# Kernel optimization log

Measured on AMD Instinct MI355X. Metric: run time of the kernel, lower is better.

## Reference

```python
import jax, jax.numpy as jnp
import numpy as np

EPS = 1e-6
N_HEADS = 128
QK_NOPE = 128
QK_ROPE = 64
KV_RANK = 512

def rmsnorm(x, gamma):
    var = jnp.mean(jnp.square(x), axis=-1, keepdims=True)
    return x * jax.lax.rsqrt(var + EPS) * gamma

def apply_rope(x, cos, sin):
    # x: [..., D], cos/sin broadcastable to x; rotate-half convention
    x1, x2 = jnp.split(x, 2, axis=-1)
    rot = jnp.concatenate([-x2, x1], axis=-1)
    return x * cos + rot * sin

def setup_inputs() -> dict:
    key = jax.random.key(0)
    ks = jax.random.split(key, 6)
    T, H = 4096, 7168
    inp = {
        "token_x": jax.random.normal(ks[0], (T, H), jnp.float32),
        "wq_a": jax.random.normal(ks[1], (H, 1536), jnp.float32) * 0.02,
        "wq_b": jax.random.normal(ks[2], (1536, N_HEADS * (QK_NOPE + QK_ROPE)), jnp.float32) * 0.02,
        "wkv": jax.random.normal(ks[3], (H, KV_RANK + QK_ROPE), jnp.float32) * 0.02,
        "rope_cos": jax.random.uniform(ks[4], (T, QK_ROPE), jnp.float32, -1.0, 1.0),
        "rope_sin": jax.random.uniform(ks[5], (T, QK_ROPE), jnp.float32, -1.0, 1.0),
        "gamma_cq": jnp.ones((1536,), jnp.float32),
        "gamma_ckv": jnp.ones((KV_RANK,), jnp.float32),
    }
    return inp

def reference(token_x, wq_a, wq_b, wkv, rope_cos, rope_sin, gamma_cq, gamma_ckv):
    T = token_x.shape[0]
    # Query path: down-proj -> RMSNorm -> up-proj -> split -> RoPE on rope part
    cq = rmsnorm(token_x @ wq_a, gamma_cq)                    # [T, 1536]
    q = (cq @ wq_b).reshape(T, N_HEADS, QK_NOPE + QK_ROPE)    # [T, H, 192]
    q_nope, q_rope = q[..., :QK_NOPE], q[..., QK_NOPE:]
    q_rope = apply_rope(q_rope, rope_cos[:, None, :], rope_sin[:, None, :])
    query = jnp.concatenate([q_nope, q_rope], axis=-1)        # [T, H, 192]
    # KV path: joint down-proj -> split latent / rope-key -> RMSNorm + RoPE
    kv = token_x @ wkv                                        # [T, 576]
    ckv = rmsnorm(kv[:, :KV_RANK], gamma_ckv)                 # [T, 512]
    k_rope = apply_rope(kv[:, KV_RANK:], rope_cos, rope_sin)  # [T, 64]
    # Pack outputs into a single array: [T, H*192 + 512 + 64]
    return jnp.concatenate([query.reshape(T, -1), ckv, k_rope], axis=-1)
```

## Files before the change

### kernel.cpp

```cpp
#include <hip/hip_runtime.h>


typedef __attribute__((ext_vector_type(8))) __bf16 bf16x8;
typedef __attribute__((ext_vector_type(4))) float f32x4;

#define OUT_LD 25152

__device__ __forceinline__ unsigned short f2bf(float f) {
  union { float f; unsigned u; } v; v.f = f;
  unsigned r = v.u + 0x7FFFu + ((v.u >> 16) & 1u);
  return (unsigned short)(r >> 16);
}

__device__ __forceinline__ void gload16(const void* g, void* l) {
  __builtin_amdgcn_global_load_lds(
      (__attribute__((address_space(1))) void*)(void*)g,
      (__attribute__((address_space(3))) void*)l, 16, 0, 0);
}

__global__ void cvt_bf16(const float* __restrict__ in, unsigned short* __restrict__ out) {
  size_t i = (size_t)blockIdx.x * 256 + threadIdx.x;
  float4 f = ((const float4*)in)[i];
  ushort4 o;
  o.x = f2bf(f.x); o.y = f2bf(f.y); o.z = f2bf(f.z); o.w = f2bf(f.w);
  ((ushort4*)out)[i] = o;
}

__global__ void transpose_cvt(const float* __restrict__ in, unsigned short* __restrict__ out,
                              int K, int N, int Npad) {
  __shared__ float tile[32][33];
  int k0 = blockIdx.x * 32, n0 = blockIdx.y * 32;
  int tx = threadIdx.x, ty = threadIdx.y;
#pragma unroll
  for (int i = 0; i < 4; ++i) {
    int k = k0 + ty + i * 8;
    int n = n0 + tx;
    tile[ty + i * 8][tx] = (n < N) ? in[(size_t)k * N + n] : 0.f;
  }
  __syncthreads();
#pragma unroll
  for (int i = 0; i < 4; ++i) {
    int n = n0 + ty + i * 8;
    int k = k0 + tx;
    if (n < Npad) out[(size_t)n * K + k] = f2bf(tile[tx][ty + i * 8]);
  }
}

__global__ __launch_bounds__(256, 2) void gemm128(
    const unsigned short* __restrict__ A, const unsigned short* __restrict__ B,
    float* __restrict__ C, int K, int ldc, int Nvalid) {
  __shared__ __attribute__((aligned(128))) unsigned short As[128 * 32];
  __shared__ __attribute__((aligned(128))) unsigned short Bs[128 * 32];
  const int tid = threadIdx.x;
  const int lane = tid & 63;
  const int wid = tid >> 6;
  const int wr = wid >> 1, wc = wid & 1;
  const int bm = blockIdx.y, bn = blockIdx.x;
  const size_t abase = (size_t)bm * 128 * K;
  const size_t bbase = (size_t)bn * 128 * K;

  f32x4 acc[4][4];
  const f32x4 zero4 = {0.f, 0.f, 0.f, 0.f};
#pragma unroll
  for (int m = 0; m < 4; ++m)
#pragma unroll
    for (int n = 0; n < 4; ++n) acc[m][n] = zero4;

  const int r0 = tid >> 2;
  const int c0 = (tid & 3) * 8;

  for (int k0 = 0; k0 < K; k0 += 32) {
    gload16(A + abase + (size_t)r0 * K + k0 + c0, As + tid * 8);
    gload16(A + abase + (size_t)(r0 + 64) * K + k0 + c0, As + (256 + tid) * 8);
    gload16(B + bbase + (size_t)r0 * K + k0 + c0, Bs + tid * 8);
    gload16(B + bbase + (size_t)(r0 + 64) * K + k0 + c0, Bs + (256 + tid) * 8);
    __syncthreads();
    bf16x8 af[4], bfr[4];
#pragma unroll
    for (int m = 0; m < 4; ++m)
      af[m] = *(const bf16x8*)(As + (wr * 64 + m * 16 + (lane & 15)) * 32 + (lane >> 4) * 8);
#pragma unroll
    for (int n = 0; n < 4; ++n)
      bfr[n] = *(const bf16x8*)(Bs + (wc * 64 + n * 16 + (lane & 15)) * 32 + (lane >> 4) * 8);
#pragma unroll
    for (int m = 0; m < 4; ++m)
#pragma unroll
      for (int n = 0; n < 4; ++n)
        acc[m][n] = __builtin_amdgcn_mfma_f32_16x16x32_bf16(af[m], bfr[n], acc[m][n], 0, 0, 0);
    __syncthreads();
  }

  const int crow0 = bm * 128 + wr * 64 + ((lane >> 4) << 2);
  const int ccol0 = bn * 128 + wc * 64 + (lane & 15);
#pragma unroll
  for (int m = 0; m < 4; ++m) {
#pragma unroll
    for (int n = 0; n < 4; ++n) {
      int col = ccol0 + n * 16;
      if (col < Nvalid) {
#pragma unroll
        for (int r = 0; r < 4; ++r) {
          int row = crow0 + m * 16 + r;
          C[(size_t)row * ldc + col] = acc[m][n][r];
        }
      }
    }
  }
}

__global__ void rmsnorm_cq(const float* __restrict__ raw, const float* __restrict__ gamma,
                           unsigned short* __restrict__ out) {
  __shared__ float red[4];
  int t = blockIdx.x, tid = threadIdx.x;
  const float* r = raw + (size_t)t * 2176;
  float v[6];
  float ss = 0.f;
#pragma unroll
  for (int i = 0; i < 6; ++i) {
    v[i] = r[tid + i * 256];
    ss += v[i] * v[i];
  }
#pragma unroll
  for (int o = 32; o > 0; o >>= 1) ss += __shfl_xor(ss, o, 64);
  if ((tid & 63) == 0) red[tid >> 6] = ss;
  __syncthreads();
  ss = red[0] + red[1] + red[2] + red[3];
  float sc = rsqrtf(ss * (1.f / 1536.f) + 1e-6f);
#pragma unroll
  for (int i = 0; i < 6; ++i)
    out[(size_t)t * 1536 + tid + i * 256] = f2bf(v[i] * sc * gamma[tid + i * 256]);
}

__global__ void kv_epi(const float* __restrict__ raw, const float* __restrict__ gamma,
                       const float* __restrict__ cs, const float* __restrict__ sn,
                       float* __restrict__ out) {
  __shared__ float red[4];
  int t = blockIdx.x, tid = threadIdx.x;
  const float* r = raw + (size_t)t * 2176 + 1536;
  float v0 = r[tid], v1 = r[tid + 256];
  float ss = v0 * v0 + v1 * v1;
#pragma unroll
  for (int o = 32; o > 0; o >>= 1) ss += __shfl_xor(ss, o, 64);
  if ((tid & 63) == 0) red[tid >> 6] = ss;
  __syncthreads();
  ss = red[0] + red[1] + red[2] + red[3];
  float sc = rsqrtf(ss * (1.f / 512.f) + 1e-6f);
  float* orow = out + (size_t)t * OUT_LD + 24576;
  orow[tid] = v0 * sc * gamma[tid];
  orow[tid + 256] = v1 * sc * gamma[tid + 256];
  if (tid < 32) {
    float a = r[512 + tid], b = r[544 + tid];
    orow[512 + tid] = a * cs[t * 64 + tid] - b * sn[t * 64 + tid];
    orow[544 + tid] = b * cs[t * 64 + 32 + tid] + a * sn[t * 64 + 32 + tid];
  }
}

__global__ void rope_q(float* __restrict__ out, const float* __restrict__ cs,
                       const float* __restrict__ sn) {
  int idx = blockIdx.x * 256 + threadIdx.x;
  int i = idx & 31;
  int h = (idx >> 5) & 127;
  int t = idx >> 12;
  float* p = out + (size_t)t * OUT_LD + h * 192 + 128;
  float a = p[i], b = p[32 + i];
  float c1 = cs[t * 64 + i], s1 = sn[t * 64 + i];
  float c2 = cs[t * 64 + 32 + i], s2 = sn[t * 64 + 32 + i];
  p[i] = a * c1 - b * s1;
  p[32 + i] = b * c2 + a * s2;
}

extern "C" void kernel_launch(void* const* d_in, const int* in_sizes, int n_in,
                              void* d_out, int out_size, void* d_ws, size_t ws_size,
                              hipStream_t stream) {
  const float* token_x = (const float*)d_in[0];
  const float* wq_a = (const float*)d_in[1];
  const float* wq_b = (const float*)d_in[2];
  const float* wkv = (const float*)d_in[3];
  const float* rope_cos = (const float*)d_in[4];
  const float* rope_sin = (const float*)d_in[5];
  const float* gamma_cq = (const float*)d_in[6];
  const float* gamma_ckv = (const float*)d_in[7];
  float* out = (float*)d_out;

  char* ws = (char*)d_ws;
  unsigned short* txb = (unsigned short*)ws;
  unsigned short* wqbT = (unsigned short*)(ws + 58720256);
  unsigned short* Bc = (unsigned short*)(ws + 134217728);
  float* raw = (float*)(ws + 165412864);
  unsigned short* cqb = (unsigned short*)(ws + 201064448);

  cvt_bf16<<<28672, 256, 0, stream>>>(token_x, txb);
  transpose_cvt<<<dim3(7168 / 32, 1536 / 32), dim3(32, 8), 0, stream>>>(wq_a, Bc, 7168, 1536, 1536);
  transpose_cvt<<<dim3(7168 / 32, 640 / 32), dim3(32, 8), 0, stream>>>(
      wkv, Bc + (size_t)1536 * 7168, 7168, 576, 640);
  transpose_cvt<<<dim3(1536 / 32, 24576 / 32), dim3(32, 8), 0, stream>>>(wq_b, wqbT, 1536, 24576, 24576);

  gemm128<<<dim3(17, 32), 256, 0, stream>>>(txb, Bc, raw, 7168, 2176, 2176);

  rmsnorm_cq<<<4096, 256, 0, stream>>>(raw, gamma_cq, cqb);
  kv_epi<<<4096, 256, 0, stream>>>(raw, gamma_ckv, rope_cos, rope_sin, out);

  gemm128<<<dim3(192, 32), 256, 0, stream>>>(cqb, wqbT, out, 1536, OUT_LD, 24576);

  rope_q<<<65536, 256, 0, stream>>>(out, rope_cos, rope_sin);
}
```

Baseline: 820.7 us.

## Replace Q up-projection GEMM with pipelined 256x256 tile kernel fusing RoPE

Adds a 512-thread GEMM kernel with 256x256 tiles, double-buffered LDS staged by direct global-to-LDS loads, XOR-swizzled LDS layout, a permuted B-row mapping and an L2-friendly block swizzle. The Q up-projection uses it, and RoPE is applied in the epilogue for column groups that hold the rope part, so the separate rope_q pass over the output goes away. The intent is higher MFMA utilisation and less global traffic. The cost is 128KB of LDS per block, which limits occupancy, plus fragile hand-written waitcnt and barrier scheduling.

```diff
diff --git a/kernel.cpp b/kernel.cpp
--- a/kernel.cpp
+++ b/kernel.cpp
@@ -44,6 +44,156 @@
     int k = k0 + tx;
     if (n < Npad) out[(size_t)n * K + k] = f2bf(tile[tx][ty + i * 8]);
   }
+}
+
+__global__ __launch_bounds__(512, 2) void gemm256(
+    const unsigned short* __restrict__ A, const unsigned short* __restrict__ B,
+    float* __restrict__ C, int K, int ldc, int Mtiles,
+    const float* __restrict__ cs, const float* __restrict__ sn, int rope) {
+  __shared__ __attribute__((aligned(128))) char lds[131072];
+  const int tid = threadIdx.x;
+  const int lane = tid & 63;
+  const int wr = (tid >> 6) >> 2;
+  const int wc = (tid >> 6) & 3;
+  const int NT = K >> 6;
+
+  const int nwg = gridDim.x;
+  const int per = nwg >> 3;
+  const int bid = blockIdx.x;
+  const int swz = (bid & 7) * per + (bid >> 3);
+  const int bm = swz % Mtiles, bn = swz / Mtiles;
+
+  const int strow = tid >> 3;
+  const int stcolb = ((tid & 7) << 4) ^ (((tid >> 5) & 1) << 5);
+  const size_t abase = (size_t)(bm * 256) * K;
+  const size_t bbase = (size_t)(bn * 256) * K;
+
+  f32x4 acc[2][2][4][2];
+  const f32x4 z4 = {0.f, 0.f, 0.f, 0.f};
+#pragma unroll
+  for (int a = 0; a < 2; ++a)
+#pragma unroll
+    for (int b = 0; b < 2; ++b)
+#pragma unroll
+      for (int c = 0; c < 4; ++c)
+#pragma unroll
+        for (int d = 0; d < 2; ++d) acc[a][b][c][d] = z4;
+
+#define STAGE_A(kt, bsel, u)                                                        \
+  do {                                                                              \
+    int row_ = (u) * 64 + strow;                                                    \
+    gload16((const char*)(A + abase + (size_t)row_ * K + (size_t)(kt) * 64) + stcolb, \
+            lds + (bsel) * 65536 + (u) * 8192 + tid * 16);                          \
+  } while (0)
+#define STAGE_B(kt, bsel, u)                                                        \
+  do {                                                                              \
+    int lrow_ = (u) * 64 + strow;                                                   \
+    int n_ = ((lrow_ >> 5) & 3) * 64 + ((lrow_ >> 7) & 1) * 32 + (lrow_ & 31);      \
+    gload16((const char*)(B + bbase + (size_t)n_ * K + (size_t)(kt) * 64) + stcolb, \
+            lds + (bsel) * 65536 + 32768 + (u) * 8192 + tid * 16);                  \
+  } while (0)
+
+  STAGE_A(0, 0, 0); STAGE_A(0, 0, 1); STAGE_A(0, 0, 2); STAGE_A(0, 0, 3);
+  STAGE_B(0, 0, 0); STAGE_B(0, 0, 1); STAGE_B(0, 0, 2); STAGE_B(0, 0, 3);
+  if (NT > 1) {
+    STAGE_A(1, 1, 0); STAGE_A(1, 1, 1);
+    STAGE_B(1, 1, 2); STAGE_B(1, 1, 3);
+    asm volatile("s_waitcnt vmcnt(4)" ::: "memory");
+  } else {
+    asm volatile("s_waitcnt vmcnt(0)" ::: "memory");
+  }
+  __builtin_amdgcn_s_barrier();
+  __builtin_amdgcn_sched_barrier(0);
+
+#define PHASE(QM, QN, STAGES)                                                        \
+  do {                                                                               \
+    const char* Lb_ = lds + buf * 65536;                                             \
+    bf16x8 af_[4][2], bb_[2][2];                                                     \
+    _Pragma("unroll") for (int mf = 0; mf < 4; ++mf)                                 \
+        _Pragma("unroll") for (int ks = 0; ks < 2; ++ks) {                           \
+      int row_ = (QM) * 128 + wr * 64 + mf * 16 + (lane & 15);                       \
+      int tb_ = row_ * 128 + ks * 64 + ((lane >> 4) << 4);                           \
+      af_[mf][ks] = *(const bf16x8*)(Lb_ + (tb_ ^ (((row_ >> 2) & 1) << 5)));        \
+    }                                                                                \
+    _Pragma("unroll") for (int nf = 0; nf < 2; ++nf)                                 \
+        _Pragma("unroll") for (int ks = 0; ks < 2; ++ks) {                           \
+      int c_ = wc * 64 + (QN) * 32 + nf * 16 + (lane & 15);                          \
+      int rr_ = ((c_ >> 5) & 1) * 128 + ((c_ >> 6) & 3) * 32 + (c_ & 31);            \
+      int tb_ = rr_ * 128 + ks * 64 + ((lane >> 4) << 4);                            \
+      bb_[nf][ks] = *(const bf16x8*)(Lb_ + 32768 + (tb_ ^ (((rr_ >> 2) & 1) << 5))); \
+    }                                                                                \
+    STAGES;                                                                          \
+    __builtin_amdgcn_s_barrier();                                                    \
+    asm volatile("s_waitcnt lgkmcnt(0)" ::: "memory");                               \
+    __builtin_amdgcn_sched_barrier(0);                                               \
+    __builtin_amdgcn_s_setprio(1);                                                   \
+    _Pragma("unroll") for (int mf = 0; mf < 4; ++mf)                                 \
+        _Pragma("unroll") for (int nf = 0; nf < 2; ++nf)                             \
+            _Pragma("unroll") for (int ks = 0; ks < 2; ++ks)                         \
+                acc[QM][QN][mf][nf] = __builtin_amdgcn_mfma_f32_16x16x32_bf16(       \
+                    af_[mf][ks], bb_[nf][ks], acc[QM][QN][mf][nf], 0, 0, 0);         \
+    __builtin_amdgcn_s_setprio(0);                                                   \
+  } while (0)
+
+  for (int t = 0; t < NT; ++t) {
+    const int buf = t & 1;
+    const int pb = buf ^ 1;
+    PHASE(0, 0, { if (t + 1 < NT) { STAGE_A(t + 1, pb, 2); STAGE_A(t + 1, pb, 3); } });
+    __builtin_amdgcn_s_barrier();
+    PHASE(0, 1, { if (t + 1 < NT) { STAGE_B(t + 1, pb, 0); STAGE_B(t + 1, pb, 1); } });
+    __builtin_amdgcn_s_barrier();
+    PHASE(1, 1, { if (t + 2 < NT) { STAGE_A(t + 2, buf, 0); STAGE_A(t + 2, buf, 1); } });
+    __builtin_amdgcn_s_barrier();
+    PHASE(1, 0, { if (t + 2 < NT) { STAGE_B(t + 2, buf, 2); STAGE_B(t + 2, buf, 3); } });
+    if (t + 2 < NT) {
+      asm volatile("s_waitcnt vmcnt(4)" ::: "memory");
+    } else {
+      asm volatile("s_waitcnt vmcnt(0)" ::: "memory");
+    }
+    __builtin_amdgcn_s_barrier();
+    __builtin_amdgcn_sched_barrier(0);
+  }
+
+  const int colbase = bn * 256 + wc * 64;
+  const int rbase = bm * 256 + wr * 64 + ((lane >> 4) << 2);
+  const bool isrope = rope && ((colbase % 192) == 128);
+  if (isrope) {
+#pragma unroll
+    for (int qm = 0; qm < 2; ++qm)
+#pragma unroll
+      for (int mf = 0; mf < 4; ++mf)
+#pragma unroll
+        for (int nf = 0; nf < 2; ++nf) {
+          int i_ = nf * 16 + (lane & 15);
+#pragma unroll
+          for (int r = 0; r < 4; ++r) {
+            int trow = rbase + qm * 128 + mf * 16 + r;
+            float c1 = cs[trow * 64 + i_], s1 = sn[trow * 64 + i_];
+            float c2 = cs[trow * 64 + 32 + i_], s2 = sn[trow * 64 + 32 + i_];
+            float a = acc[qm][0][mf][nf][r], b = acc[qm][1][mf][nf][r];
+            C[(size_t)trow * ldc + colbase + i_] = a * c1 - b * s1;
+            C[(size_t)trow * ldc + colbase + 32 + i_] = b * c2 + a * s2;
+          }
+        }
+  } else {
+#pragma unroll
+    for (int qm = 0; qm < 2; ++qm)
+#pragma unroll
+      for (int qn = 0; qn < 2; ++qn)
+#pragma unroll
+        for (int mf = 0; mf < 4; ++mf)
+#pragma unroll
+          for (int nf = 0; nf < 2; ++nf)
+#pragma unroll
+            for (int r = 0; r < 4; ++r) {
+              int trow = rbase + qm * 128 + mf * 16 + r;
+              C[(size_t)trow * ldc + colbase + qn * 32 + nf * 16 + (lane & 15)] =
+                  acc[qm][qn][mf][nf][r];
+            }
+  }
+#undef PHASE
+#undef STAGE_A
+#undef STAGE_B
 }
 
 __global__ __launch_bounds__(256, 2) void gemm128(
@@ -155,20 +305,6 @@
   }
 }
 
-__global__ void rope_q(float* __restrict__ out, const float* __restrict__ cs,
-                       const float* __restrict__ sn) {
-  int idx = blockIdx.x * 256 + threadIdx.x;
-  int i = idx & 31;
-  int h = (idx >> 5) & 127;
-  int t = idx >> 12;
-  float* p = out + (size_t)t * OUT_LD + h * 192 + 128;
-  float a = p[i], b = p[32 + i];
-  float c1 = cs[t * 64 + i], s1 = sn[t * 64 + i];
-  float c2 = cs[t * 64 + 32 + i], s2 = sn[t * 64 + 32 + i];
-  p[i] = a * c1 - b * s1;
-  p[32 + i] = b * c2 + a * s2;
-}
-
 extern "C" void kernel_launch(void* const* d_in, const int* in_sizes, int n_in,
                               void* d_out, int out_size, void* d_ws, size_t ws_size,
                               hipStream_t stream) {
@@ -200,7 +336,5 @@
   rmsnorm_cq<<<4096, 256, 0, stream>>>(raw, gamma_cq, cqb);
   kv_epi<<<4096, 256, 0, stream>>>(raw, gamma_ckv, rope_cos, rope_sin, out);
 
-  gemm128<<<dim3(192, 32), 256, 0, stream>>>(cqb, wqbT, out, 1536, OUT_LD, 24576);
-
-  rope_q<<<65536, 256, 0, stream>>>(out, rope_cos, rope_sin);
-}
+  gemm256<<<1536, 512, 0, stream>>>(cqb, wqbT, out, 1536, OUT_LD, 16, rope_cos, rope_sin, 1);
+}
```

Measured after the change: 799.5 us. 1.03x faster.
